# Kernel tuning notes

Measured on AMD Instinct MI355X. Metric: run time of the kernel, lower is better.

The kernel has to match this reference:

```python
import jax, jax.numpy as jnp
import numpy as np

DIM_IN = 32
DIM_OUT = 32
DIM_X = 64   # dim_internal
DIM_NL = 32
EPS_Q = 1e-4      # eps in default Q
TOL = 1e-3        # pos_def_tol
D22_EPS = 1.0     # d22_epsilon


def _model_param(X, Y, B2, C2, D12, D22_L, D22_U, D21, gamma):
    """Faithful port of REN_IQC_gamma._update_model_param (QR_fun=None, dim_in==dim_out)."""
    g = gamma[0, 0]
    Q = -EPS_Q * jnp.eye(DIM_OUT)
    R = -2.0 * g * jnp.eye(DIM_IN)
    S = jnp.eye(DIM_OUT, DIM_IN)
    # D22 = base + sym + skew (dim_in == dim_out)
    D22 = (g + D22_EPS) * jnp.eye(DIM_OUT, DIM_IN) + D22_L.T @ D22_L + (D22_U - D22_U.T)
    SD = S @ D22
    R_cal = R + SD + SD.T + D22.T @ Q @ D22
    R_cal_inv = jnp.linalg.inv(R_cal)
    M = D22.T @ Q + S
    C2_cal = M @ C2                      # (dim_in, dim_x)
    D21_cal = M @ D21 - D12.T            # (dim_in, dim_nl)
    vec_r = jnp.concatenate([C2_cal.T, D21_cal.T, B2], axis=0)   # (2*dim_x+dim_nl, dim_in)
    psi_r = vec_r @ R_cal_inv @ vec_r.T
    vec_q = jnp.concatenate([C2.T, D21.T, jnp.zeros((DIM_X, DIM_OUT), X.dtype)], axis=0)
    psi_q = vec_q @ Q @ vec_q.T
    n = 2 * DIM_X + DIM_NL
    H = X.T @ X + TOL * jnp.eye(n) + psi_r - psi_q
    i1, i2 = DIM_X, DIM_X + DIM_NL
    H11 = H[:i1, :i1]
    H21 = H[i1:i2, :i1]
    H22 = H[i1:i2, i1:i2]
    H31 = H[i2:, :i1]
    H32 = H[i2:, i1:i2]
    H33 = H[i2:, i2:]
    E = 0.5 * (H11 + H33 + Y - Y.T)
    E_inv = jnp.linalg.inv(E)
    Lam = 0.5 * jnp.diag(H22)            # Lambda (dim_nl,)
    D11 = -jnp.tril(H22, k=-1)           # strictly lower triangular
    C1 = -H21
    Fm = H31
    B1 = H32
    return Fm, B1, E_inv, Lam, D11, C1, D22


def reference(u_in, x0, X, Y, B2, C2, D12, D22_L, D22_U, D21, gamma):
    # Parameters are constant across time steps, so the per-step recompute in the
    # torch code collapses to a single evaluation with identical math.
    Fm, B1, E_inv, Lam, D11, C1, D22 = _model_param(X, Y, B2, C2, D12, D22_L, D22_U, D21, gamma)
    B = u_in.shape[0]
    nl_idx = jnp.arange(DIM_NL)

    def step(x, u_t):                    # x: (B, DIM_X), u_t: (B, DIM_IN)
        a = x @ C1.T + u_t @ D12.T       # (B, DIM_NL), constant part of v

        def inner(w, i):                 # forward substitution over strictly-lower D11
            v = a[:, i] + w @ D11[i]     # (B,)
            w = w.at[:, i].set(jnp.tanh(v / Lam[i]))
            return w, None

        w, _ = jax.lax.scan(inner, jnp.zeros((B, DIM_NL), u_in.dtype), nl_idx)
        x_new = (x @ Fm.T + w @ B1.T + u_t @ B2.T) @ E_inv.T
        y_t = x_new @ C2.T + w @ D21.T + u_t @ D22.T
        return x_new, y_t

    u_time = jnp.swapaxes(u_in, 0, 1)    # (T, B, DIM_IN)
    _, ys = jax.lax.scan(step, x0[:, 0, :], u_time)
    return jnp.swapaxes(ys, 0, 1)        # (B, T, DIM_OUT)


def setup_inputs() -> dict:
    key = jax.random.key(0)
    ks = jax.random.split(key, 10)
    std = 0.5
    n = 2 * DIM_X + DIM_NL
    B, T = 2048, 256
    return {
        "u_in": jax.random.normal(ks[0], (B, T, DIM_IN), jnp.float32),
        "x0": jax.random.normal(ks[1], (B, 1, DIM_X), jnp.float32),
        "X": jax.random.normal(ks[2], (n, n), jnp.float32) * std,
        "Y": jax.random.normal(ks[3], (DIM_X, DIM_X), jnp.float32) * std,
        "B2": jax.random.normal(ks[4], (DIM_X, DIM_IN), jnp.float32) * std,
        "C2": jax.random.normal(ks[5], (DIM_OUT, DIM_X), jnp.float32) * std,
        "D12": jax.random.normal(ks[6], (DIM_NL, DIM_IN), jnp.float32) * std,
        "D22_L": jax.random.normal(ks[7], (DIM_IN, DIM_IN), jnp.float32) * std,
        "D22_U": jax.random.normal(ks[8], (DIM_OUT, DIM_IN), jnp.float32) * std,
        "D21": jnp.zeros((DIM_OUT, DIM_NL), jnp.float32),   # registered buffer, fixed zero
        "gamma": jax.random.normal(ks[9], (1, 1), jnp.float32) * 3.0,
    }
```

## Files before the change

### kernel.cpp

```cpp
#include <hip/hip_runtime.h>
#include <math.h>

#define EPS_Q 1e-4
#define TOLC  1e-3

#define OFF_D22   0
#define OFF_RINV  1024
#define OFF_VR    2048
#define OFF_T1    7168
#define OFF_H     12288
#define OFF_E     37888
#define OFF_EI    41984
#define OFF_TMP   46080
#define OFF_TMP2  50176
#define D_END     54272

__global__ __launch_bounds__(1024, 1) void prep1(
    const float* __restrict__ B2, const float* __restrict__ C2,
    const float* __restrict__ D12, const float* __restrict__ L,
    const float* __restrict__ U, const float* __restrict__ D21,
    const float* __restrict__ gam, double* __restrict__ wsd)
{
  __shared__ double aug[32][65];
  __shared__ double sFac[32];
  __shared__ int sPiv;
  const int tid = threadIdx.x;
  const double g = (double)gam[0];
  double* D22d = wsd + OFF_D22;

  for (int idx = tid; idx < 1024; idx += 1024) {
    int i = idx >> 5, j = idx & 31;
    double s = (i == j) ? (g + 1.0) : 0.0;
    for (int k = 0; k < 32; ++k) s += (double)L[k*32+i] * (double)L[k*32+j];
    s += (double)U[i*32+j] - (double)U[j*32+i];
    D22d[idx] = s;
  }
  __syncthreads();
  for (int idx = tid; idx < 1024; idx += 1024) {
    int i = idx >> 5, j = idx & 31;
    double s = (i == j) ? (-2.0 * g) : 0.0;
    s += D22d[i*32+j] + D22d[j*32+i];
    double q = 0.0;
    for (int k = 0; k < 32; ++k) q += D22d[k*32+i] * D22d[k*32+j];
    aug[i][j] = s - EPS_Q * q;
    aug[i][32+j] = (i == j) ? 1.0 : 0.0;
  }
  __syncthreads();
  for (int k = 0; k < 32; ++k) {
    if (tid < 64) {
      float mv = -1.f; int mi = k;
      if (tid < 32 && tid >= k) { mv = (float)fabs(aug[tid][k]); mi = tid; }
      #pragma unroll
      for (int o = 32; o; o >>= 1) {
        float ov = __shfl_xor(mv, o); int oi = __shfl_xor(mi, o);
        if (ov > mv) { mv = ov; mi = oi; }
      }
      if (tid == 0) sPiv = mi;
    }
    __syncthreads();
    int p = sPiv;
    if (p != k) for (int c = tid; c < 64; c += 1024) { double t1 = aug[k][c]; aug[k][c] = aug[p][c]; aug[p][c] = t1; }
    __syncthreads();
    double pinv = 1.0 / aug[k][k];
    if (tid < 32 && tid != k) sFac[tid] = aug[tid][k];
    __syncthreads();
    for (int c = tid; c < 64; c += 1024) aug[k][c] *= pinv;
    __syncthreads();
    for (int idx = tid; idx < 2048; idx += 1024) {
      int r = idx >> 6, c = idx & 63;
      if (r != k) aug[r][c] -= sFac[r] * aug[k][c];
    }
    __syncthreads();
  }
  double* Rinv = wsd + OFF_RINV;
  for (int idx = tid; idx < 1024; idx += 1024) Rinv[idx] = aug[idx >> 5][32 + (idx & 31)];

  double* vr = wsd + OFF_VR;
  for (int idx = tid; idx < 64*32; idx += 1024) {
    int p = idx >> 5, k = idx & 31;
    double q = 0.0;
    for (int m = 0; m < 32; ++m) q += D22d[m*32+k] * (double)C2[m*64+p];
    vr[p*32+k] = (double)C2[k*64+p] - EPS_Q * q;
  }
  for (int idx = tid; idx < 32*32; idx += 1024) {
    int p = idx >> 5, k = idx & 31;
    double q = 0.0;
    for (int m = 0; m < 32; ++m) q += D22d[m*32+k] * (double)D21[m*32+p];
    vr[(64+p)*32+k] = (double)D21[k*32+p] - EPS_Q * q - (double)D12[p*32+k];
  }
  for (int idx = tid; idx < 64*32; idx += 1024) {
    int p = idx >> 5, k = idx & 31;
    vr[(96+p)*32+k] = (double)B2[p*32+k];
  }
  __syncthreads();
  double* T1 = wsd + OFF_T1;
  for (int idx = tid; idx < 160*32; idx += 1024) {
    int p = idx >> 5, k2 = idx & 31;
    double s = 0.0;
    for (int k = 0; k < 32; ++k) s += vr[p*32+k] * Rinv[k*32+k2];
    T1[idx] = s;
  }
}

__global__ __launch_bounds__(256, 1) void prep2(
    const float* __restrict__ X, const float* __restrict__ C2,
    const float* __restrict__ D21, double* __restrict__ wsd)
{
  const double* vr = wsd + OFF_VR;
  const double* T1 = wsd + OFF_T1;
  double* H = wsd + OFF_H;
  int bi = blockIdx.x / 10, bj = blockIdx.x % 10;
  int i = bi*16 + (threadIdx.x >> 4);
  int j = bj*16 + (threadIdx.x & 15);
  double s = (i == j) ? TOLC : 0.0;
  for (int k = 0; k < 160; ++k) s += (double)X[k*160+i] * (double)X[k*160+j];
  double pr = 0.0;
  for (int k = 0; k < 32; ++k) pr += T1[i*32+k] * vr[j*32+k];
  s += pr;
  if (i < 96 && j < 96) {
    double vq = 0.0;
    for (int k = 0; k < 32; ++k) {
      double a = (i < 64) ? (double)C2[k*64+i] : (double)D21[k*32+(i-64)];
      double b = (j < 64) ? (double)C2[k*64+j] : (double)D21[k*32+(j-64)];
      vq += a*b;
    }
    s += EPS_Q * vq;
  }
  H[i*160+j] = s;
}

__global__ __launch_bounds__(1024, 1) void prep3(
    const float* __restrict__ Y, const float* __restrict__ B2,
    const float* __restrict__ C2, const float* __restrict__ D12,
    const float* __restrict__ D21, double* __restrict__ wsd)
{
  __shared__ float aug[64][130];
  __shared__ float sFac[64];
  __shared__ int sPiv;
  const int tid = threadIdx.x;
  double* H   = wsd + OFF_H;
  double* Ed  = wsd + OFF_E;
  double* Ei  = wsd + OFF_EI;
  double* Tm  = wsd + OFF_TMP;
  double* Tm2 = wsd + OFF_TMP2;
  double* D22d = wsd + OFF_D22;
  float* fb = (float*)(wsd + D_END);
  const double KS = 2.8853900817779268;

  for (int idx = tid; idx < 4096; idx += 1024) {
    int i = idx >> 6, j = idx & 63;
    double e = 0.5*(H[i*160+j] + H[(96+i)*160+(96+j)] + (double)Y[i*64+j] - (double)Y[j*64+i]);
    Ed[idx] = e;
    aug[i][j] = (float)e;
    aug[i][64+j] = (i == j) ? 1.f : 0.f;
  }
  __syncthreads();
  for (int k = 0; k < 64; ++k) {
    if (tid < 64) {
      float mv = -1.f; int mi = k;
      if (tid >= k) { mv = fabsf(aug[tid][k]); mi = tid; }
      #pragma unroll
      for (int o = 32; o; o >>= 1) {
        float ov = __shfl_xor(mv, o); int oi = __shfl_xor(mi, o);
        if (ov > mv) { mv = ov; mi = oi; }
      }
      if (tid == 0) sPiv = mi;
    }
    __syncthreads();
    int p = sPiv;
    if (p != k) for (int c = tid; c < 128; c += 1024) { float t1 = aug[k][c]; aug[k][c] = aug[p][c]; aug[p][c] = t1; }
    __syncthreads();
    float pinv = 1.0f / aug[k][k];
    if (tid < 64 && tid != k) sFac[tid] = aug[tid][k];
    __syncthreads();
    for (int c = tid; c < 128; c += 1024) aug[k][c] *= pinv;
    __syncthreads();
    for (int idx = tid; idx < 64*128; idx += 1024) {
      int r = idx >> 7, c = idx & 127;
      if (r != k) aug[r][c] -= sFac[r] * aug[k][c];
    }
    __syncthreads();
  }
  for (int idx = tid; idx < 4096; idx += 1024) Ei[idx] = (double)aug[idx >> 6][64 + (idx & 63)];
  __syncthreads();
  for (int it = 0; it < 2; ++it) {
    for (int idx = tid; idx < 4096; idx += 1024) {
      int i = idx >> 6, j = idx & 63;
      double s = (i == j) ? 2.0 : 0.0;
      for (int k = 0; k < 64; ++k) s -= Ed[i*64+k] * Ei[k*64+j];
      Tm[idx] = s;
    }
    __syncthreads();
    for (int idx = tid; idx < 4096; idx += 1024) {
      int i = idx >> 6, j = idx & 63;
      double s = 0.0;
      for (int k = 0; k < 64; ++k) s += Ei[i*64+k] * Tm[k*64+j];
      Tm2[idx] = s;
    }
    __syncthreads();
    for (int idx = tid; idx < 4096; idx += 1024) Ei[idx] = Tm2[idx];
    __syncthreads();
  }
  for (int idx = tid; idx < 64*128; idx += 1024) {
    int r = idx >> 7, col = idx & 127;
    double s = 0.0;
    if (col < 64)       { for (int k = 0; k < 64; ++k) s += Ei[r*64+k] * H[(96+k)*160 + col]; }
    else if (col < 96)  { int jj = col-64; for (int k = 0; k < 64; ++k) s += Ei[r*64+k] * H[(96+k)*160 + 64 + jj]; }
    else                { int jj = col-96; for (int k = 0; k < 64; ++k) s += Ei[r*64+k] * (double)B2[k*32+jj]; }
    fb[((col >> 2)*64 + r)*4 + (col & 3)] = (float)s;
  }
  for (int idx = tid; idx < 32*128; idx += 1024) {
    int r = idx >> 7, col = idx & 127;
    float v;
    if (col < 64)      v = C2[r*64 + col];
    else if (col < 96) v = D21[r*32 + (col-64)];
    else               v = (float)D22d[r*32 + (col-96)];
    fb[8192 + ((col >> 2)*32 + r)*4 + (col & 3)] = v;
  }
  for (int idx = tid; idx < 1024; idx += 1024) {
    int i = idx >> 5, j = idx & 31;
    double li = 2.0 / H[(64+i)*160 + 64+i];
    fb[12288 + idx] = (j < i) ? (float)(-H[(64+i)*160 + 64+j] * li * KS) : 0.f;
  }
  for (int idx = tid; idx < 32*96; idx += 1024) {
    int r = idx / 96, j = idx % 96;
    double li = 2.0 / H[(64+r)*160 + 64+r];
    double v = (j < 64) ? (-H[(64+r)*160 + j] * li) : ((double)D12[r*32 + (j-64)] * li);
    fb[13312 + idx] = (float)(v * KS);
  }
}

__device__ __forceinline__ float frcp(float x) {
#if __has_builtin(__builtin_amdgcn_rcpf)
  return __builtin_amdgcn_rcpf(x);
#else
  return 1.0f / x;
#endif
}
__device__ __forceinline__ float hsum4(float4 a) { return (a.x + a.y) + (a.z + a.w); }

#define PIN(x) asm volatile("" : "+v"(x))
__global__ __launch_bounds__(256, 1) void ren_main(
    const float* __restrict__ u_in, const float* __restrict__ x0,
    const double* __restrict__ wsd, float* __restrict__ out)
{
  __shared__ __align__(16) float sW[8192];
  __shared__ __align__(16) float sXU[4][132];
  const float* fb = (const float*)(wsd + D_END);
  const int tid = threadIdx.x;
  {
    const float4* g4 = (const float4*)fb;
    float4* s4 = (float4*)sW;
    for (int i = tid; i < 1024; i += 256) s4[i] = g4[2048 + i];
    for (int i = tid; i < 768; i += 256) {
      int r2 = i / 24, ch = i % 24;
      s4[1024 + ch*32 + r2] = g4[3328 + i];
    }
    if (tid < 256) s4[1792 + tid] = g4[1792 + tid];
  }
  const int wv = tid >> 6, l = tid & 63;
  const int r = l & 31, lh = l >> 5;
  const int e = blockIdx.x * 4 + wv;
  float* xu = &sXU[wv][0];

  float4 wx[28];
  {
    const float4* WxG = (const float4*)fb;
    #pragma unroll
    for (int c = 0; c < 28; ++c) wx[c] = WxG[(c << 6) + l];
  }
  float d11[32];
  {
    const float4* DG = (const float4*)(fb + 12288);
    #pragma unroll
    for (int c = 0; c < 8; ++c) {
      float4 dv = DG[r*8 + c];
      d11[4*c+0] = dv.x; d11[4*c+1] = dv.y; d11[4*c+2] = dv.z; d11[4*c+3] = dv.w;
    }
  }
  #pragma unroll
  for (int c = 0; c < 28; ++c) {
    PIN(wx[c].x); PIN(wx[c].y); PIN(wx[c].z); PIN(wx[c].w);
  }
  #pragma unroll
  for (int j = 0; j < 32; ++j) PIN(d11[j]);

  xu[l] = x0[(size_t)e*64 + l];
  xu[96 + r] = u_in[(size_t)e*8192 + r];
  __syncthreads();

  const float4* xu4  = (const float4*)xu;
  const float4* WyT4 = (const float4*)sW;
  const float4* WaT4 = (const float4*)sW + 1024;
  const float4* sWx4 = (const float4*)sW + 1792;
  const float* uG = u_in + (size_t)e * 8192;
  float* oG = out + (size_t)e * 8192;

#define FMA4(A, W, XV) \
  A.x = fmaf(W.x, XV.x, A.x); A.y = fmaf(W.y, XV.y, A.y); \
  A.z = fmaf(W.z, XV.z, A.z); A.w = fmaf(W.w, XV.w, A.w);

  for (int t = 0; t < 256; ++t) {
    const int tn = (t < 255) ? (t + 1) : 255;
    float unext = uG[tn*32 + r];
    float4 sA = make_float4(0.f, 0.f, 0.f, 0.f);
    #pragma unroll
    for (int c = 0; c < 12; ++c) {
      int ch = lh*12 + c;
      int xi = (ch < 16) ? ch : (ch + 8);
      float4 xv = xu4[xi]; float4 wv4 = WaT4[ch*32 + r];
      FMA4(sA, wv4, xv)
    }
    float a = hsum4(sA);
    a += __shfl_xor(a, 32);
    float4 P4 = make_float4(0.f, 0.f, 0.f, 0.f);
    #pragma unroll
    for (int c = 0; c < 16; ++c) { float4 xv = xu4[c]; FMA4(P4, wx[c], xv) }
    #pragma unroll
    for (int c = 24; c < 28; ++c) { float4 xv = xu4[c]; FMA4(P4, wx[c], xv) }
    #pragma unroll
    for (int c = 28; c < 32; ++c) { float4 xv = xu4[c]; float4 wv4 = sWx4[((c - 28) << 6) + l]; FMA4(P4, wv4, xv) }
    float4 Q4 = make_float4(0.f, 0.f, 0.f, 0.f);
    #pragma unroll
    for (int c = 0; c < 4; ++c) {
      int ch = 24 + lh*4 + c;
      float4 xv = xu4[ch]; float4 wv4 = WyT4[(ch << 5) + r];
      FMA4(Q4, wv4, xv)
    }
    float v = a;
    #pragma unroll
    for (int j = 0; j < 31; ++j) {
      float E = __builtin_exp2f(v);
      float w = fmaf(-2.f, frcp(E + 1.f), 1.f);
      float b = __int_as_float(__builtin_amdgcn_readlane(__float_as_int(w), j));
      v = fmaf(d11[j], b, v);
    }
    float Ef = __builtin_exp2f(v);
    float myw = fmaf(-2.f, frcp(Ef + 1.f), 1.f);
    xu[64 + r] = myw;
    #pragma unroll
    for (int c = 16; c < 24; ++c) { float4 xv = xu4[c]; FMA4(P4, wx[c], xv) }
    xu[l] = hsum4(P4);
    #pragma unroll
    for (int c = 0; c < 12; ++c) {
      int ch = lh*12 + c;
      float4 xv = xu4[ch]; float4 wv4 = WyT4[(ch << 5) + r];
      FMA4(Q4, wv4, xv)
    }
    float y = hsum4(Q4);
    y += __shfl_xor(y, 32);
    if (l < 32) oG[t*32 + l] = y;
    xu[96 + r] = unext;
  }
#undef FMA4
}
#undef PIN

extern "C" void kernel_launch(void* const* d_in, const int* in_sizes, int n_in,
                              void* d_out, int out_size, void* d_ws, size_t ws_size,
                              hipStream_t stream)
{
  const float* u_in = (const float*)d_in[0];
  const float* x0   = (const float*)d_in[1];
  const float* X    = (const float*)d_in[2];
  const float* Y    = (const float*)d_in[3];
  const float* B2   = (const float*)d_in[4];
  const float* C2   = (const float*)d_in[5];
  const float* D12  = (const float*)d_in[6];
  const float* L    = (const float*)d_in[7];
  const float* U    = (const float*)d_in[8];
  const float* D21  = (const float*)d_in[9];
  const float* gam  = (const float*)d_in[10];
  double* wsd = (double*)d_ws;
  float* out = (float*)d_out;

  hipLaunchKernelGGL(prep1, dim3(1), dim3(1024), 0, stream, B2, C2, D12, L, U, D21, gam, wsd);
  hipLaunchKernelGGL(prep2, dim3(100), dim3(256), 0, stream, X, C2, D21, wsd);
  hipLaunchKernelGGL(prep3, dim3(1), dim3(1024), 0, stream, Y, B2, C2, D12, D21, wsd);
  hipLaunchKernelGGL(ren_main, dim3(512), dim3(256), 0, stream, u_in, x0, wsd, out);
}
```

Before: 1.358 ms.

## Split each batch element's recurrence across two specialized wavefronts per step

Each block now runs 512 threads. For every batch element, one wavefront handles the nonlinear forward substitution and the output, and a partner wavefront computes the state update and prefetches the next input. The Wx weights move from registers into shared memory, and the u slots are double-buffered so the two roles can overlap within a time step. In exchange, every step now has two block-wide barriers, and the weights are read from LDS instead of registers.

```diff
diff --git a/kernel.cpp b/kernel.cpp
--- a/kernel.cpp
+++ b/kernel.cpp
@@ -240,117 +240,114 @@
 __device__ __forceinline__ float hsum4(float4 a) { return (a.x + a.y) + (a.z + a.w); }
 
 #define PIN(x) asm volatile("" : "+v"(x))
-__global__ __launch_bounds__(256, 1) void ren_main(
+__global__ __launch_bounds__(512, 1) void ren_main(
     const float* __restrict__ u_in, const float* __restrict__ x0,
     const double* __restrict__ wsd, float* __restrict__ out)
 {
-  __shared__ __align__(16) float sW[8192];
-  __shared__ __align__(16) float sXU[4][132];
+  __shared__ __align__(16) float sW[15360 + 4*168];
   const float* fb = (const float*)(wsd + D_END);
   const int tid = threadIdx.x;
   {
     const float4* g4 = (const float4*)fb;
     float4* s4 = (float4*)sW;
-    for (int i = tid; i < 1024; i += 256) s4[i] = g4[2048 + i];
-    for (int i = tid; i < 768; i += 256) {
+    for (int i = tid; i < 3072; i += 512) s4[i] = g4[i];
+    for (int i = tid; i < 768; i += 512) {
       int r2 = i / 24, ch = i % 24;
-      s4[1024 + ch*32 + r2] = g4[3328 + i];
-    }
-    if (tid < 256) s4[1792 + tid] = g4[1792 + tid];
+      s4[3072 + ch*32 + r2] = g4[3328 + i];
+    }
   }
   const int wv = tid >> 6, l = tid & 63;
+  const int p = wv & 3;
+  const bool isA = (wv < 4);
   const int r = l & 31, lh = l >> 5;
-  const int e = blockIdx.x * 4 + wv;
-  float* xu = &sXU[wv][0];
-
-  float4 wx[28];
-  {
-    const float4* WxG = (const float4*)fb;
-    #pragma unroll
-    for (int c = 0; c < 28; ++c) wx[c] = WxG[(c << 6) + l];
-  }
+  const int e = blockIdx.x * 4 + p;
+  float* xu = sW + 15360 + p * 168;
+  const float4* xu4 = (const float4*)xu;
+  const float4* Wx4 = (const float4*)sW;
+  const float4* Wy4 = (const float4*)sW + 2048;
+  const float4* Wa4 = (const float4*)sW + 3072;
+  const float* uG = u_in + (size_t)e * 8192;
+  float* oG = out + (size_t)e * 8192;
+
   float d11[32];
-  {
+  if (isA) {
     const float4* DG = (const float4*)(fb + 12288);
     #pragma unroll
     for (int c = 0; c < 8; ++c) {
       float4 dv = DG[r*8 + c];
       d11[4*c+0] = dv.x; d11[4*c+1] = dv.y; d11[4*c+2] = dv.z; d11[4*c+3] = dv.w;
     }
-  }
-  #pragma unroll
-  for (int c = 0; c < 28; ++c) {
-    PIN(wx[c].x); PIN(wx[c].y); PIN(wx[c].z); PIN(wx[c].w);
-  }
-  #pragma unroll
-  for (int j = 0; j < 32; ++j) PIN(d11[j]);
-
-  xu[l] = x0[(size_t)e*64 + l];
-  xu[96 + r] = u_in[(size_t)e*8192 + r];
-  __syncthreads();
-
-  const float4* xu4  = (const float4*)xu;
-  const float4* WyT4 = (const float4*)sW;
-  const float4* WaT4 = (const float4*)sW + 1024;
-  const float4* sWx4 = (const float4*)sW + 1792;
-  const float* uG = u_in + (size_t)e * 8192;
-  float* oG = out + (size_t)e * 8192;
+    #pragma unroll
+    for (int j = 0; j < 32; ++j) PIN(d11[j]);
+    xu[l] = x0[(size_t)e*64 + l];
+    if (l < 32) xu[96 + r] = uG[r];
+  }
+  __syncthreads();
 
 #define FMA4(A, W, XV) \
   A.x = fmaf(W.x, XV.x, A.x); A.y = fmaf(W.y, XV.y, A.y); \
   A.z = fmaf(W.z, XV.z, A.z); A.w = fmaf(W.w, XV.w, A.w);
 
+  float4 acc;
+  float un = 0.f;
   for (int t = 0; t < 256; ++t) {
-    const int tn = (t < 255) ? (t + 1) : 255;
-    float unext = uG[tn*32 + r];
-    float4 sA = make_float4(0.f, 0.f, 0.f, 0.f);
-    #pragma unroll
-    for (int c = 0; c < 12; ++c) {
-      int ch = lh*12 + c;
-      int xi = (ch < 16) ? ch : (ch + 8);
-      float4 xv = xu4[xi]; float4 wv4 = WaT4[ch*32 + r];
-      FMA4(sA, wv4, xv)
-    }
-    float a = hsum4(sA);
-    a += __shfl_xor(a, 32);
-    float4 P4 = make_float4(0.f, 0.f, 0.f, 0.f);
-    #pragma unroll
-    for (int c = 0; c < 16; ++c) { float4 xv = xu4[c]; FMA4(P4, wx[c], xv) }
-    #pragma unroll
-    for (int c = 24; c < 28; ++c) { float4 xv = xu4[c]; FMA4(P4, wx[c], xv) }
-    #pragma unroll
-    for (int c = 28; c < 32; ++c) { float4 xv = xu4[c]; float4 wv4 = sWx4[((c - 28) << 6) + l]; FMA4(P4, wv4, xv) }
-    float4 Q4 = make_float4(0.f, 0.f, 0.f, 0.f);
-    #pragma unroll
-    for (int c = 0; c < 4; ++c) {
-      int ch = 24 + lh*4 + c;
-      float4 xv = xu4[ch]; float4 wv4 = WyT4[(ch << 5) + r];
-      FMA4(Q4, wv4, xv)
-    }
-    float v = a;
-    #pragma unroll
-    for (int j = 0; j < 31; ++j) {
-      float E = __builtin_exp2f(v);
-      float w = fmaf(-2.f, frcp(E + 1.f), 1.f);
-      float b = __int_as_float(__builtin_amdgcn_readlane(__float_as_int(w), j));
-      v = fmaf(d11[j], b, v);
-    }
-    float Ef = __builtin_exp2f(v);
-    float myw = fmaf(-2.f, frcp(Ef + 1.f), 1.f);
-    xu[64 + r] = myw;
-    #pragma unroll
-    for (int c = 16; c < 24; ++c) { float4 xv = xu4[c]; FMA4(P4, wx[c], xv) }
-    xu[l] = hsum4(P4);
-    #pragma unroll
-    for (int c = 0; c < 12; ++c) {
-      int ch = lh*12 + c;
-      float4 xv = xu4[ch]; float4 wv4 = WyT4[(ch << 5) + r];
-      FMA4(Q4, wv4, xv)
-    }
-    float y = hsum4(Q4);
-    y += __shfl_xor(y, 32);
-    if (l < 32) oG[t*32 + l] = y;
-    xu[96 + r] = unext;
+    const int ub = t & 1;
+    acc = make_float4(0.f, 0.f, 0.f, 0.f);
+    if (isA) {
+      float4 sA = make_float4(0.f, 0.f, 0.f, 0.f);
+      #pragma unroll
+      for (int c = 0; c < 12; ++c) {
+        int ch = lh*12 + c;
+        int xi = (ch < 16) ? ch : (ch + 8 + 8*ub);
+        float4 xv = xu4[xi]; float4 wv4 = Wa4[ch*32 + r];
+        FMA4(sA, wv4, xv)
+      }
+      float a = hsum4(sA);
+      a += __shfl_xor(a, 32);
+      float v = a;
+      #pragma unroll
+      for (int j = 0; j < 31; ++j) {
+        float E = __builtin_exp2f(v);
+        float w = fmaf(-2.f, frcp(E + 1.f), 1.f);
+        float b = __int_as_float(__builtin_amdgcn_readlane(__float_as_int(w), j));
+        v = fmaf(d11[j], b, v);
+      }
+      float Ef = __builtin_exp2f(v);
+      xu[64 + r] = fmaf(-2.f, frcp(Ef + 1.f), 1.f);
+      #pragma unroll
+      for (int c = 0; c < 8; ++c) {
+        int ch = (c < 4) ? (16 + lh*4 + c) : (24 + lh*4 + (c - 4));
+        int xi = (ch < 24) ? ch : (ch + 8*ub);
+        float4 xv = xu4[xi]; float4 wv4 = Wy4[(ch << 5) + r];
+        FMA4(acc, wv4, xv)
+      }
+    } else {
+      const int tn = (t < 255) ? (t + 1) : 255;
+      un = uG[tn*32 + r];
+      #pragma unroll
+      for (int c = 0; c < 16; ++c) { float4 xv = xu4[c]; FMA4(acc, Wx4[(c << 6) + l], xv) }
+      #pragma unroll
+      for (int c = 24; c < 32; ++c) { float4 xv = xu4[c + 8*ub]; FMA4(acc, Wx4[(c << 6) + l], xv) }
+    }
+    __syncthreads();
+    if (!isA) {
+      #pragma unroll
+      for (int c = 16; c < 24; ++c) { float4 xv = xu4[c]; FMA4(acc, Wx4[(c << 6) + l], xv) }
+      xu[l] = hsum4(acc);
+      if (l < 32) xu[96 + 32*(ub ^ 1) + r] = un;
+    }
+    __syncthreads();
+    if (isA) {
+      #pragma unroll
+      for (int c = 0; c < 8; ++c) {
+        int ch = lh*8 + c;
+        float4 xv = xu4[ch]; float4 wv4 = Wy4[(ch << 5) + r];
+        FMA4(acc, wv4, xv)
+      }
+      float y = hsum4(acc);
+      y += __shfl_xor(y, 32);
+      if (l < 32) oG[t*32 + l] = y;
+    }
   }
 #undef FMA4
 }
@@ -377,5 +374,5 @@
   hipLaunchKernelGGL(prep1, dim3(1), dim3(1024), 0, stream, B2, C2, D12, L, U, D21, gam, wsd);
   hipLaunchKernelGGL(prep2, dim3(100), dim3(256), 0, stream, X, C2, D21, wsd);
   hipLaunchKernelGGL(prep3, dim3(1), dim3(1024), 0, stream, Y, B2, C2, D12, D21, wsd);
-  hipLaunchKernelGGL(ren_main, dim3(512), dim3(256), 0, stream, u_in, x0, wsd, out);
-}
+  hipLaunchKernelGGL(ren_main, dim3(512), dim3(512), 0, stream, u_in, x0, wsd, out);
+}
```

Measured after the change: 1.863 ms. +37.2%, slower.
